# Performance work log

Hardware: AMD Instinct MI355X
Metric: run time of the kernel (lower is better)

Reference implementation:

```python
import jax, jax.numpy as jnp
import numpy as np

N_A, N_B, N_C = 64, 128, 128
D_IN, D_H, N_HEADS = 256, 32, 4


def setup_inputs() -> dict:
    key = jax.random.key(0)
    ks = jax.random.split(key, 8)
    s_in = 1.0 / np.sqrt(D_IN)
    s_fc = 1.0 / np.sqrt(D_H * N_HEADS)
    return {
        "H_a": jax.random.normal(ks[0], (N_A, D_IN), jnp.float32),
        "H_b": jax.random.normal(ks[1], (N_B, D_IN), jnp.float32),
        "H_c": jax.random.normal(ks[2], (N_C, D_IN), jnp.float32),
        "W_q": jax.random.normal(ks[3], (D_IN, D_H * N_HEADS), jnp.float32) * s_in,
        "W_k": jax.random.normal(ks[4], (D_IN, D_H * N_HEADS), jnp.float32) * s_in,
        "W_v": jax.random.normal(ks[5], (D_IN, D_H * N_HEADS), jnp.float32) * s_in,
        "fc_w": jax.random.normal(ks[6], (D_H * N_HEADS, 1), jnp.float32) * s_fc,
        "fc_b": jnp.zeros((1,), jnp.float32),
    }


def reference(H_a, H_b, H_c, W_q, W_k, W_v, fc_w, fc_b):
    Na, Nb, Nc = H_a.shape[0], H_b.shape[0], H_c.shape[0]
    Q = (H_a @ W_q).reshape(Na, N_HEADS, D_H)   # [Na,H,d]
    Kb = (H_b @ W_k).reshape(Nb, N_HEADS, D_H)  # [Nb,H,d]
    Kc = (H_c @ W_k).reshape(Nc, N_HEADS, D_H)  # [Nc,H,d]
    Vb = (H_b @ W_v).reshape(Nb, N_HEADS, D_H)
    Vc = (H_c @ W_v).reshape(Nc, N_HEADS, D_H)
    scale = 1.0 / np.sqrt(D_H)
    s_ab = jnp.einsum('ahd,bhd->ahb', Q, Kb) * scale        # [Na,H,Nb]
    s_ac = jnp.einsum('ahd,chd->ahc', Q, Kc) * scale        # [Na,H,Nc]
    s_bc = jnp.einsum('bhd,chd->hbc', Kb, Kc) * scale       # [H,Nb,Nc]
    # 3-way fused score: [Na,H,Nb,Nc]
    scores = s_ab[:, :, :, None] + s_ac[:, :, None, :] + s_bc[None]
    alpha = jax.nn.softmax(scores.reshape(Na, N_HEADS, Nb * Nc), axis=-1)
    alpha = alpha.reshape(Na, N_HEADS, Nb, Nc)
    # V sum broadcast: [1,H,Nb,Nc,d]
    v_sum = (jnp.transpose(Vb, (1, 0, 2))[None, :, :, None, :]
             + jnp.transpose(Vc, (1, 0, 2))[None, :, None, :, :])
    context = alpha[..., None] * v_sum                      # [Na,H,Nb,Nc,d]
    # faithful row-major reinterpretation (matches torch .view)
    context = context.reshape(Na, Nb, Nc, N_HEADS * D_H)
    out = jax.nn.sigmoid(context @ fc_w + fc_b)[..., 0]     # [Na,Nb,Nc]
    return out
```

## Files before the change

### kernel.cpp

```cpp
#include <hip/hip_runtime.h>
#include <math.h>

#define N_A 64
#define N_B 128
#define N_C 128
#define D_IN 256
#define D_H 32
#define NHEADS 4
#define DMODEL (D_H * NHEADS)

#define OFF_Q    0
#define OFF_KB   (OFF_Q   + N_A*DMODEL)
#define OFF_KC   (OFF_KB  + N_B*DMODEL)
#define OFF_VB   (OFF_KC  + N_C*DMODEL)
#define OFF_VC   (OFF_VB  + N_B*DMODEL)
#define OFF_PB   (OFF_VC  + N_C*DMODEL)
#define OFF_PC   (OFF_PB  + N_B*NHEADS*4)

#define SCALE 0.17677669529663687f

__device__ __forceinline__ float dot4(float4 a, float4 b) {
  return fmaf(a.x, b.x, fmaf(a.y, b.y, fmaf(a.z, b.z, a.w * b.w)));
}

__device__ __forceinline__ int kswz(int row, int d) {
  return (row * 32 + d) ^ (((row >> 3) & 7) << 2);
}

__global__ __launch_bounds__(1024) void k1(
    const float* __restrict__ Ha, const float* __restrict__ Hb,
    const float* __restrict__ Hc, const float* __restrict__ Wq,
    const float* __restrict__ Wk, const float* __restrict__ Wv,
    const float* __restrict__ fcw, float* __restrict__ ws) {
  __shared__ float part[2 * 4 * 2 * 128];
  __shared__ float rowsL[4][128];
  const int t   = threadIdx.x;
  const int tid = blockIdx.x * 1024 + t;
  const int r2  = tid >> 9;
  const int ks  = (t >> 7) & 3;
  const int col = t & 127;
  const int rl  = t >> 9;

  const float* X; const float* W; float* Y; int r;
  {
    const int row = r2 * 2;
    if (row < 64)       { X = Ha; W = Wq; Y = ws + OFF_Q;  r = row; }
    else if (row < 192) { X = Hb; W = Wk; Y = ws + OFF_KB; r = row - 64; }
    else if (row < 320) { X = Hc; W = Wk; Y = ws + OFF_KC; r = row - 192; }
    else if (row < 448) { X = Hb; W = Wv; Y = ws + OFF_VB; r = row - 320; }
    else                { X = Hc; W = Wv; Y = ws + OFF_VC; r = row - 448; }
  }
  const float* x0 = X + r * D_IN;
  const float* x1 = x0 + D_IN;
  const int i0 = ks * 64;
  float acc0 = 0.0f, acc1 = 0.0f;
  #pragma unroll 8
  for (int i = 0; i < 64; ++i) {
    const float w = W[(i0 + i) * DMODEL + col];
    acc0 = fmaf(x0[i0 + i], w, acc0);
    acc1 = fmaf(x1[i0 + i], w, acc1);
  }
  part[((rl * 4 + ks) * 2 + 0) * 128 + col] = acc0;
  part[((rl * 4 + ks) * 2 + 1) * 128 + col] = acc1;
  __syncthreads();
  if (ks == 0) {
    float f0 = 0.0f, f1 = 0.0f;
    #pragma unroll
    for (int k = 0; k < 4; ++k) {
      f0 += part[((rl * 4 + k) * 2 + 0) * 128 + col];
      f1 += part[((rl * 4 + k) * 2 + 1) * 128 + col];
    }
    Y[r * DMODEL + col]       = f0;
    Y[(r + 1) * DMODEL + col] = f1;
    rowsL[rl * 2 + 0][col] = f0;
    rowsL[rl * 2 + 1][col] = f1;
  }
  __syncthreads();

  if (t < 64) {
    const int lr = t >> 4, e = t & 15, hh = e >> 2, kk = e & 3;
    const int row = blockIdx.x * 4 + lr;
    if (row >= 320) {
      float s = 0.0f;
      #pragma unroll
      for (int d = 0; d < D_H; ++d)
        s = fmaf(rowsL[lr][hh * D_H + d], fcw[kk * D_H + d], s);
      if (row < 448) {
        const int b = row - 320;
        ws[OFF_PB + (b * 4 + hh) * 4 + kk] = s;
      } else {
        const int cc = row - 448;
        if (kk == (cc & 3)) ws[OFF_PC + hh * N_C + cc] = s;
      }
    }
  }
}

__global__ __launch_bounds__(512) void k2(
    const float* __restrict__ ws, const float* __restrict__ fcb,
    float* __restrict__ out) {
  __shared__ float KbL[128 * 32];
  __shared__ float KcL[128 * 32];
  __shared__ float EbcL[128 * 128];
  __shared__ float qaL[32];
  __shared__ float EabL[128], EacL[128], UL[128];
  __shared__ float red[4];

  const int t = threadIdx.x;
  const int a = blockIdx.x >> 2;
  const int h = blockIdx.x & 3;

  {
    const int d = t & 31, r0 = t >> 5;
    #pragma unroll
    for (int p = 0; p < 8; ++p) {
      const int r = r0 + p * 16;
      KbL[kswz(r, d)] = ws[OFF_KB + r * DMODEL + h * D_H + d];
      KcL[kswz(r, d)] = ws[OFF_KC + r * DMODEL + h * D_H + d];
    }
    if (t < 32) qaL[t] = ws[OFF_Q + a * DMODEL + h * D_H + t];
  }
  __syncthreads();

  {
    const int r = t >> 2, part = t & 3, d0 = part * 8;
    const float4 q0 = *(const float4*)&qaL[d0];
    const float4 q1 = *(const float4*)&qaL[d0 + 4];
    float4 x0 = *(const float4*)&KbL[kswz(r, d0)];
    float4 x1 = *(const float4*)&KbL[kswz(r, d0 + 4)];
    float s = dot4(q0, x0) + dot4(q1, x1);
    s += __shfl_xor(s, 1); s += __shfl_xor(s, 2);
    if (part == 0) EabL[r] = __expf(s * SCALE);
    x0 = *(const float4*)&KcL[kswz(r, d0)];
    x1 = *(const float4*)&KcL[kswz(r, d0 + 4)];
    s = dot4(q0, x0) + dot4(q1, x1);
    s += __shfl_xor(s, 1); s += __shfl_xor(s, 2);
    if (part == 0) EacL[r] = __expf(s * SCALE);
  }

  if (t < 256) {
    const int b0 = (t >> 4) * 8, c0 = (t & 15) * 8;
    float acc[8][8];
    #pragma unroll
    for (int i = 0; i < 8; ++i)
      #pragma unroll
      for (int j = 0; j < 8; ++j) acc[i][j] = 0.0f;

    #pragma unroll
    for (int d0 = 0; d0 < 32; d0 += 4) {
      float4 cv[8];
      #pragma unroll
      for (int j = 0; j < 8; ++j) cv[j] = *(const float4*)&KcL[kswz(c0 + j, d0)];
      #pragma unroll
      for (int i = 0; i < 8; ++i) {
        const float4 bv = *(const float4*)&KbL[kswz(b0 + i, d0)];
        #pragma unroll
        for (int j = 0; j < 8; ++j) acc[i][j] += dot4(bv, cv[j]);
      }
    }
    #pragma unroll
    for (int i = 0; i < 8; ++i)
      #pragma unroll
      for (int j = 0; j < 8; ++j)
        EbcL[(b0 + i) * 128 + c0 + j] = __expf(acc[i][j] * SCALE);
  }
  __syncthreads();

  {
    const int b = t >> 2, part = t & 3, cb = part * 32;
    float s = 0.0f;
    #pragma unroll
    for (int k = 0; k < 8; ++k) {
      const float4 e  = *(const float4*)&EbcL[b * 128 + cb + k * 4];
      const float4 av = *(const float4*)&EacL[cb + k * 4];
      s += dot4(e, av);
    }
    s += __shfl_xor(s, 1); s += __shfl_xor(s, 2);
    if (part == 0) UL[b] = s;
  }
  __syncthreads();

  if (t < 128) {
    float v = EabL[t] * UL[t];
    #pragma unroll
    for (int o = 32; o > 0; o >>= 1) v += __shfl_down(v, o, 64);
    if ((t & 63) == 0) red[t >> 6] = v;
  }
  __syncthreads();
  if (t == 0) red[2] = 1.0f / (red[0] + red[1]);
  __syncthreads();
  const float zi = red[2];
  const float fb = fcb[0];

  #pragma unroll
  for (int q = 0; q < 2; ++q) {
    const int qid   = t + q * 512;
    const int b_loc = qid >> 5;
    const int c0v   = (qid & 31) * 4;
    const int b     = h * 32 + b_loc;
    const int bb    = (b_loc << 2) | (c0v >> 5);
    const int base  = (c0v & 31) << 2;

    const float eabz  = EabL[bb] * zi;
    const float4 ebc4 = *(const float4*)&EbcL[bb * 128 + base];
    const float4 eac4 = *(const float4*)&EacL[base];
    const float4 pb4  = *(const float4*)(ws + OFF_PB + bb * 16 + h * 4);
    const float4 pcx4 = *(const float4*)(ws + OFF_PC + h * N_C + base);

    float accv = eac4.x * (ebc4.x * (pb4.x + pcx4.x));
    accv = fmaf(eac4.y, ebc4.y * (pb4.y + pcx4.y), accv);
    accv = fmaf(eac4.z, ebc4.z * (pb4.z + pcx4.z), accv);
    accv = fmaf(eac4.w, ebc4.w * (pb4.w + pcx4.w), accv);
    const float x = fmaf(accv, eabz, fb);

    float4 res;
    res.x = 1.0f / (1.0f + __expf(-x));
    float rr[4];
    rr[0] = res.x;
    {
    }
    #pragma unroll
    for (int j = 1; j < 4; ++j) {
      const int c    = c0v + j;
      const int bbj  = (b_loc << 2) | (c >> 5);
      const int bsj  = (c & 31) << 2;
      const float eabzj  = EabL[bbj] * zi;
      const float4 e4 = *(const float4*)&EbcL[bbj * 128 + bsj];
      const float4 a4 = *(const float4*)&EacL[bsj];
      const float4 p4 = *(const float4*)(ws + OFF_PB + bbj * 16 + h * 4);
      const float4 x4 = *(const float4*)(ws + OFF_PC + h * N_C + bsj);
      float av = a4.x * (e4.x * (p4.x + x4.x));
      av = fmaf(a4.y, e4.y * (p4.y + x4.y), av);
      av = fmaf(a4.z, e4.z * (p4.z + x4.z), av);
      av = fmaf(a4.w, e4.w * (p4.w + x4.w), av);
      const float xj = fmaf(av, eabzj, fb);
      rr[j] = 1.0f / (1.0f + __expf(-xj));
    }
    res.x = rr[0]; res.y = rr[1]; res.z = rr[2]; res.w = rr[3];
    *(float4*)(out + a * (N_B * N_C) + b * N_C + c0v) = res;
  }
}

extern "C" void kernel_launch(void* const* d_in, const int* in_sizes, int n_in,
                              void* d_out, int out_size, void* d_ws, size_t ws_size,
                              hipStream_t stream) {
  const float* Ha  = (const float*)d_in[0];
  const float* Hb  = (const float*)d_in[1];
  const float* Hc  = (const float*)d_in[2];
  const float* Wq  = (const float*)d_in[3];
  const float* Wk  = (const float*)d_in[4];
  const float* Wv  = (const float*)d_in[5];
  const float* fcw = (const float*)d_in[6];
  const float* fcb = (const float*)d_in[7];
  float* out = (float*)d_out;
  float* ws  = (float*)d_ws;

  k1<<<144, 1024, 0, stream>>>(Ha, Hb, Hc, Wq, Wk, Wv, fcw, ws);
  k2<<<256, 512, 0, stream>>>(ws, fcb, out);
}
```

Baseline: 26.33 us.

## Swizzle Ebc shared layout, stage fc partials in LDS, split k1 blocks

Changes k1 to launch 288 blocks of 512 threads, one row pair per block, and narrows the fc-projection tail to the threads that actually need it. In k2 the exp(Kb·Kc) tile gets an XOR-swizzled shared layout and is written with float4 stores, and the wave-to-tile mapping of the 8x8 outer-product tiles is changed, both to cut LDS bank conflicts. The row-sum pass now uses 128 threads with no shuffles. The PB/PC fc partials are preloaded into LDS so the output loop avoids repeated global loads. The cost is extra shared memory and a less parallel reduction step.

```diff
diff --git a/kernel.cpp b/kernel.cpp
--- a/kernel.cpp
+++ b/kernel.cpp
@@ -27,19 +27,21 @@
   return (row * 32 + d) ^ (((row >> 3) & 7) << 2);
 }
 
-__global__ __launch_bounds__(1024) void k1(
+__device__ __forceinline__ int ebx(int b, int c) {
+  return b * 128 + (c ^ (((b ^ (b >> 3)) & 7) << 2));
+}
+
+__global__ __launch_bounds__(512) void k1(
     const float* __restrict__ Ha, const float* __restrict__ Hb,
     const float* __restrict__ Hc, const float* __restrict__ Wq,
     const float* __restrict__ Wk, const float* __restrict__ Wv,
     const float* __restrict__ fcw, float* __restrict__ ws) {
-  __shared__ float part[2 * 4 * 2 * 128];
-  __shared__ float rowsL[4][128];
+  __shared__ float part[4][2][128];
+  __shared__ float rowsL[2][128];
   const int t   = threadIdx.x;
-  const int tid = blockIdx.x * 1024 + t;
-  const int r2  = tid >> 9;
-  const int ks  = (t >> 7) & 3;
+  const int r2  = blockIdx.x;
+  const int ks  = t >> 7;
   const int col = t & 127;
-  const int rl  = t >> 9;
 
   const float* X; const float* W; float* Y; int r;
   {
@@ -60,38 +62,41 @@
     acc0 = fmaf(x0[i0 + i], w, acc0);
     acc1 = fmaf(x1[i0 + i], w, acc1);
   }
-  part[((rl * 4 + ks) * 2 + 0) * 128 + col] = acc0;
-  part[((rl * 4 + ks) * 2 + 1) * 128 + col] = acc1;
+  part[ks][0][col] = acc0;
+  part[ks][1][col] = acc1;
   __syncthreads();
   if (ks == 0) {
     float f0 = 0.0f, f1 = 0.0f;
     #pragma unroll
-    for (int k = 0; k < 4; ++k) {
-      f0 += part[((rl * 4 + k) * 2 + 0) * 128 + col];
-      f1 += part[((rl * 4 + k) * 2 + 1) * 128 + col];
-    }
+    for (int k = 0; k < 4; ++k) { f0 += part[k][0][col]; f1 += part[k][1][col]; }
     Y[r * DMODEL + col]       = f0;
     Y[(r + 1) * DMODEL + col] = f1;
-    rowsL[rl * 2 + 0][col] = f0;
-    rowsL[rl * 2 + 1][col] = f1;
-  }
-  __syncthreads();
-
-  if (t < 64) {
-    const int lr = t >> 4, e = t & 15, hh = e >> 2, kk = e & 3;
-    const int row = blockIdx.x * 4 + lr;
-    if (row >= 320) {
+    rowsL[0][col] = f0;
+    rowsL[1][col] = f1;
+  }
+  __syncthreads();
+
+  const int row0 = r2 * 2;
+  if (row0 >= 320 && row0 < 448) {
+    if (t < 32) {
+      const int lr = t >> 4, e = t & 15, hh = e >> 2, kk = e & 3;
+      const int b = row0 - 320 + lr;
       float s = 0.0f;
       #pragma unroll
       for (int d = 0; d < D_H; ++d)
         s = fmaf(rowsL[lr][hh * D_H + d], fcw[kk * D_H + d], s);
-      if (row < 448) {
-        const int b = row - 320;
-        ws[OFF_PB + (b * 4 + hh) * 4 + kk] = s;
-      } else {
-        const int cc = row - 448;
-        if (kk == (cc & 3)) ws[OFF_PC + hh * N_C + cc] = s;
-      }
+      ws[OFF_PB + (b * 4 + hh) * 4 + kk] = s;
+    }
+  } else if (row0 >= 448) {
+    if (t < 8) {
+      const int lr = t >> 2, hh = t & 3;
+      const int cc = row0 - 448 + lr;
+      const int kk = cc & 3;
+      float s = 0.0f;
+      #pragma unroll
+      for (int d = 0; d < D_H; ++d)
+        s = fmaf(rowsL[lr][hh * D_H + d], fcw[kk * D_H + d], s);
+      ws[OFF_PC + hh * N_C + cc] = s;
     }
   }
 }
@@ -104,6 +109,8 @@
   __shared__ float EbcL[128 * 128];
   __shared__ float qaL[32];
   __shared__ float EabL[128], EacL[128], UL[128];
+  __shared__ float pbL[128 * 4];
+  __shared__ float pcxL[128];
   __shared__ float red[4];
 
   const int t = threadIdx.x;
@@ -119,27 +126,32 @@
       KcL[kswz(r, d)] = ws[OFF_KC + r * DMODEL + h * D_H + d];
     }
     if (t < 32) qaL[t] = ws[OFF_Q + a * DMODEL + h * D_H + t];
+    pbL[t] = ws[OFF_PB + (t >> 2) * 16 + h * 4 + (t & 3)];
+    if (t < 128) pcxL[t] = ws[OFF_PC + h * N_C + t];
   }
   __syncthreads();
 
   {
-    const int r = t >> 2, part = t & 3, d0 = part * 8;
+    const int r = t >> 2, p = t & 3, d0 = p * 8;
     const float4 q0 = *(const float4*)&qaL[d0];
     const float4 q1 = *(const float4*)&qaL[d0 + 4];
     float4 x0 = *(const float4*)&KbL[kswz(r, d0)];
     float4 x1 = *(const float4*)&KbL[kswz(r, d0 + 4)];
     float s = dot4(q0, x0) + dot4(q1, x1);
     s += __shfl_xor(s, 1); s += __shfl_xor(s, 2);
-    if (part == 0) EabL[r] = __expf(s * SCALE);
+    if (p == 0) EabL[r] = __expf(s * SCALE);
     x0 = *(const float4*)&KcL[kswz(r, d0)];
     x1 = *(const float4*)&KcL[kswz(r, d0 + 4)];
     s = dot4(q0, x0) + dot4(q1, x1);
     s += __shfl_xor(s, 1); s += __shfl_xor(s, 2);
-    if (part == 0) EacL[r] = __expf(s * SCALE);
+    if (p == 0) EacL[r] = __expf(s * SCALE);
   }
 
   if (t < 256) {
-    const int b0 = (t >> 4) * 8, c0 = (t & 15) * 8;
+    const int w  = t >> 6;
+    const int bt = (t & 7) | ((w & 1) << 3);
+    const int ct = ((t >> 3) & 7) | ((w >> 1) << 3);
+    const int b0 = bt * 8, c0 = ct * 8;
     float acc[8][8];
     #pragma unroll
     for (int i = 0; i < 8; ++i)
@@ -159,24 +171,27 @@
       }
     }
     #pragma unroll
-    for (int i = 0; i < 8; ++i)
-      #pragma unroll
-      for (int j = 0; j < 8; ++j)
-        EbcL[(b0 + i) * 128 + c0 + j] = __expf(acc[i][j] * SCALE);
-  }
-  __syncthreads();
-
-  {
-    const int b = t >> 2, part = t & 3, cb = part * 32;
+    for (int i = 0; i < 8; ++i) {
+      float4 lo, hi;
+      lo.x = __expf(acc[i][0] * SCALE); lo.y = __expf(acc[i][1] * SCALE);
+      lo.z = __expf(acc[i][2] * SCALE); lo.w = __expf(acc[i][3] * SCALE);
+      hi.x = __expf(acc[i][4] * SCALE); hi.y = __expf(acc[i][5] * SCALE);
+      hi.z = __expf(acc[i][6] * SCALE); hi.w = __expf(acc[i][7] * SCALE);
+      *(float4*)&EbcL[ebx(b0 + i, c0)]     = lo;
+      *(float4*)&EbcL[ebx(b0 + i, c0 + 4)] = hi;
+    }
+  }
+  __syncthreads();
+
+  if (t < 128) {
     float s = 0.0f;
-    #pragma unroll
-    for (int k = 0; k < 8; ++k) {
-      const float4 e  = *(const float4*)&EbcL[b * 128 + cb + k * 4];
-      const float4 av = *(const float4*)&EacL[cb + k * 4];
-      s += dot4(e, av);
-    }
-    s += __shfl_xor(s, 1); s += __shfl_xor(s, 2);
-    if (part == 0) UL[b] = s;
+    #pragma unroll 8
+    for (int k = 0; k < 32; ++k) {
+      const float4 e = *(const float4*)&EbcL[ebx(t, 4 * k)];
+      const float4 v = *(const float4*)&EacL[4 * k];
+      s += dot4(e, v);
+    }
+    UL[t] = s;
   }
   __syncthreads();
 
@@ -199,44 +214,26 @@
     const int c0v   = (qid & 31) * 4;
     const int b     = h * 32 + b_loc;
     const int bb    = (b_loc << 2) | (c0v >> 5);
-    const int base  = (c0v & 31) << 2;
-
-    const float eabz  = EabL[bb] * zi;
-    const float4 ebc4 = *(const float4*)&EbcL[bb * 128 + base];
-    const float4 eac4 = *(const float4*)&EacL[base];
-    const float4 pb4  = *(const float4*)(ws + OFF_PB + bb * 16 + h * 4);
-    const float4 pcx4 = *(const float4*)(ws + OFF_PC + h * N_C + base);
-
-    float accv = eac4.x * (ebc4.x * (pb4.x + pcx4.x));
-    accv = fmaf(eac4.y, ebc4.y * (pb4.y + pcx4.y), accv);
-    accv = fmaf(eac4.z, ebc4.z * (pb4.z + pcx4.z), accv);
-    accv = fmaf(eac4.w, ebc4.w * (pb4.w + pcx4.w), accv);
-    const float x = fmaf(accv, eabz, fb);
-
-    float4 res;
-    res.x = 1.0f / (1.0f + __expf(-x));
+    const int base0 = (c0v & 31) << 2;
+
+    const float eabz = EabL[bb] * zi;
+    const float4 pb4 = *(const float4*)&pbL[bb * 4];
+
     float rr[4];
-    rr[0] = res.x;
-    {
-    }
-    #pragma unroll
-    for (int j = 1; j < 4; ++j) {
-      const int c    = c0v + j;
-      const int bbj  = (b_loc << 2) | (c >> 5);
-      const int bsj  = (c & 31) << 2;
-      const float eabzj  = EabL[bbj] * zi;
-      const float4 e4 = *(const float4*)&EbcL[bbj * 128 + bsj];
-      const float4 a4 = *(const float4*)&EacL[bsj];
-      const float4 p4 = *(const float4*)(ws + OFF_PB + bbj * 16 + h * 4);
-      const float4 x4 = *(const float4*)(ws + OFF_PC + h * N_C + bsj);
-      float av = a4.x * (e4.x * (p4.x + x4.x));
-      av = fmaf(a4.y, e4.y * (p4.y + x4.y), av);
-      av = fmaf(a4.z, e4.z * (p4.z + x4.z), av);
-      av = fmaf(a4.w, e4.w * (p4.w + x4.w), av);
-      const float xj = fmaf(av, eabzj, fb);
+    #pragma unroll
+    for (int j = 0; j < 4; ++j) {
+      const int bs = base0 + 4 * j;
+      const float4 e4 = *(const float4*)&EbcL[ebx(bb, bs)];
+      const float4 a4 = *(const float4*)&EacL[bs];
+      const float4 x4 = *(const float4*)&pcxL[bs];
+      float av = a4.x * (e4.x * (pb4.x + x4.x));
+      av = fmaf(a4.y, e4.y * (pb4.y + x4.y), av);
+      av = fmaf(a4.z, e4.z * (pb4.z + x4.z), av);
+      av = fmaf(a4.w, e4.w * (pb4.w + x4.w), av);
+      const float xj = fmaf(av, eabz, fb);
       rr[j] = 1.0f / (1.0f + __expf(-xj));
     }
-    res.x = rr[0]; res.y = rr[1]; res.z = rr[2]; res.w = rr[3];
+    float4 res; res.x = rr[0]; res.y = rr[1]; res.z = rr[2]; res.w = rr[3];
     *(float4*)(out + a * (N_B * N_C) + b * N_C + c0v) = res;
   }
 }
@@ -255,6 +252,6 @@
   float* out = (float*)d_out;
   float* ws  = (float*)d_ws;
 
-  k1<<<144, 1024, 0, stream>>>(Ha, Hb, Hc, Wq, Wk, Wv, fcw, ws);
+  k1<<<288, 512, 0, stream>>>(Ha, Hb, Hc, Wq, Wk, Wv, fcw, ws);
   k2<<<256, 512, 0, stream>>>(ws, fcb, out);
 }
```

Result: faster. 25.25 us (-4.1%).
